# Optimization experiments

Hardware: AMD Instinct MI355X
Metric: run time of the kernel (lower is better)

The kernel has to match this reference:

```python
import jax, jax.numpy as jnp
import numpy as np

NUM_GRAPHS = 16


def gat_layer(x, src, dst, n, W, a_s, a_d, b):
    # PyG GATConv, concat=False (mean over heads), negative_slope=0.2
    H, C = a_s.shape
    h = (x @ W).reshape(x.shape[0], H, C)            # [N,H,C]
    es = jnp.einsum('nhc,hc->nh', h, a_s)            # alpha_src per node
    ed = jnp.einsum('nhc,hc->nh', h, a_d)            # alpha_dst per node
    e = jax.nn.leaky_relu(es[src] + ed[dst], 0.2)    # [E,H]
    m = jax.ops.segment_max(e, dst, num_segments=n)
    m = jnp.where(jnp.isfinite(m), m, 0.0)
    p = jnp.exp(e - m[dst])
    denom = jax.ops.segment_sum(p, dst, num_segments=n)
    alpha = p / (denom[dst] + 1e-16)                 # segment softmax over in-edges
    out = jax.ops.segment_sum(h[src] * alpha[..., None], dst, num_segments=n)  # [N,H,C]
    return out.mean(axis=1) + b


def _forward(x, edge_index, batch,
             W_e0, a_s_e0, a_d_e0, b_e0, W_e1, a_s_e1, a_d_e1, b_e1,
             W_d0, a_s_d0, a_d_d0, b_d0, W_d1, a_s_d1, a_d_d1, b_d1,
             g_w1, g_b1, g_w2, g_b2):
    n = x.shape[0]
    loop = jnp.arange(n, dtype=edge_index.dtype)     # PyG add_self_loops=True
    src = jnp.concatenate([edge_index[0], loop])
    dst = jnp.concatenate([edge_index[1], loop])
    # encoder (dropout inert in eval)
    h = jax.nn.relu(gat_layer(x, src, dst, n, W_e0, a_s_e0, a_d_e0, b_e0))
    h = gat_layer(h, src, dst, n, W_e1, a_s_e1, a_d_e1, b_e1)
    # GlobalAttention pooling: gate MLP -> segment softmax over graphs -> scatter sum
    gate = (jax.nn.relu(h @ g_w1 + g_b1) @ g_w2 + g_b2)[:, 0]   # [N]
    gm = jax.ops.segment_max(gate, batch, num_segments=NUM_GRAPHS)
    gm = jnp.where(jnp.isfinite(gm), gm, 0.0)
    p = jnp.exp(gate - gm[batch])
    att = p / (jax.ops.segment_sum(p, batch, num_segments=NUM_GRAPHS)[batch] + 1e-16)
    pooled = jax.ops.segment_sum(att[:, None] * h, batch, num_segments=NUM_GRAPHS)
    h = pooled[batch]                                # broadcast pooled back to nodes
    # decoder (heads=1)
    h = jax.nn.relu(gat_layer(h, src, dst, n, W_d0, a_s_d0, a_d_d0, b_d0))
    return gat_layer(h, src, dst, n, W_d1, a_s_d1, a_d_d1, b_d1)


def setup_inputs() -> dict:
    key = jax.random.key(0)
    ks = jax.random.split(key, 24)
    N, E, Din, H, C = 50000, 250000, 128, 8, 64
    def w(k, shape, fan_in):
        return (jax.random.normal(k, shape, jnp.float32) / np.sqrt(fan_in)).astype(jnp.float32)
    return {
        'x': jax.random.normal(ks[0], (N, Din), jnp.float32),
        'edge_index': jax.random.randint(ks[1], (2, E), 0, N, dtype=jnp.int32),
        'batch': jnp.sort(jax.random.randint(ks[2], (N,), 0, NUM_GRAPHS, dtype=jnp.int32)),
        'W_e0': w(ks[3], (Din, H * C), Din), 'a_s_e0': w(ks[4], (H, C), C), 'a_d_e0': w(ks[5], (H, C), C), 'b_e0': w(ks[6], (C,), C),
        'W_e1': w(ks[7], (C, H * C), C), 'a_s_e1': w(ks[8], (H, C), C), 'a_d_e1': w(ks[9], (H, C), C), 'b_e1': w(ks[10], (C,), C),
        'W_d0': w(ks[11], (C, C), C), 'a_s_d0': w(ks[12], (1, C), C), 'a_d_d0': w(ks[13], (1, C), C), 'b_d0': w(ks[14], (C,), C),
        'W_d1': w(ks[15], (C, Din), C), 'a_s_d1': w(ks[16], (1, Din), Din), 'a_d_d1': w(ks[17], (1, Din), Din), 'b_d1': w(ks[18], (Din,), Din),
        'g_w1': w(ks[19], (C, C), C), 'g_b1': w(ks[20], (C,), C), 'g_w2': w(ks[21], (C, 1), C), 'g_b2': w(ks[22], (1,), C),
    }


def reference(x, edge_index, batch,
              W_e0, a_s_e0, a_d_e0, b_e0, W_e1, a_s_e1, a_d_e1, b_e1,
              W_d0, a_s_d0, a_d_d0, b_d0, W_d1, a_s_d1, a_d_d1, b_d1,
              g_w1, g_b1, g_w2, g_b2):
    return _forward(x, edge_index, batch,
                    W_e0, a_s_e0, a_d_e0, b_e0, W_e1, a_s_e1, a_d_e1, b_e1,
                    W_d0, a_s_d0, a_d_d0, b_d0, W_d1, a_s_d1, a_d_d1, b_d1,
                    g_w1, g_b1, g_w2, g_b2)
```

## Files before the change

### kernel.cpp

```cpp
#include <hip/hip_runtime.h>
#include <hip/hip_fp16.h>
#include <math.h>

#define TB 256

typedef _Float16 half8v __attribute__((ext_vector_type(8)));
typedef float float4v __attribute__((ext_vector_type(4)));

static __device__ __forceinline__ int edge_src(const int* ei, int E, int e) {
    return (e < E) ? ei[e] : (e - E);
}
static __device__ __forceinline__ int edge_dst(const int* ei, int E, int e) {
    return (e < E) ? ei[E + e] : (e - E);
}

__global__ void csr_count(const int* __restrict__ ei, int E, int Etot, int* __restrict__ cnt) {
    int e = blockIdx.x * blockDim.x + threadIdx.x;
    if (e >= Etot) return;
    atomicAdd(&cnt[edge_dst(ei, E, e)], 1);
}

__global__ __launch_bounds__(256) void scan_phase1(const int* __restrict__ cnt,
                                                   int* __restrict__ incl,
                                                   int* __restrict__ bsum, int n) {
// ... 20 lines not shown
        __syncthreads();
    }
    if (t < nb) bsum[t] = v;
}

__global__ __launch_bounds__(256) void scan_phase3(const int* __restrict__ incl,
                                                   const int* __restrict__ bsum,
                                                   int* __restrict__ off, int n) {
    int i = blockIdx.x * 256 + threadIdx.x;
    if (i < n) off[i + 1] = incl[i] + (blockIdx.x ? bsum[blockIdx.x - 1] : 0);
    if (i == 0) off[0] = 0;
}

__global__ void csr_fill(const int* __restrict__ ei, int E, int Etot,
                         const int* __restrict__ off, int* __restrict__ cur,
                         int* __restrict__ esrc) {
    int e = blockIdx.x * blockDim.x + threadIdx.x;
    if (e >= Etot) return;
    int d = edge_dst(ei, E, e);
    int pos = atomicAdd(&cur[d], 1);
    esrc[off[d] + pos] = edge_src(ei, E, e);
}

__global__ void prep_weights(const float* __restrict__ W_e0, const float* __restrict__ g_w1,
                             const float* __restrict__ W_e1, const float* __restrict__ W_d1,
                             __half* __restrict__ wt_e0, __half* __restrict__ wt_g1,
                             __half* __restrict__ wst_e1, __half* __restrict__ wst_d1) {
    int i = blockIdx.x * blockDim.x + threadIdx.x;
    if (i < 65536) {
        int nn = i / 128, kk = i % 128;
        wt_e0[i] = __float2half(W_e0[kk * 512 + nn]);
    } else if (i < 69632) {
        int j = i - 65536;
        int nn = j / 64, kk = j % 64;
        wt_g1[j] = __float2half(g_w1[kk * 64 + nn]);
    } else if (i < 102400) {
        int j = i - 69632;
        int c = j / 512, rem = j % 512;
        int h = rem / 64, k = rem % 64;
        wst_e1[j] = __float2half(W_e1[(size_t)k * 512 + h * 64 + c]);
    } else if (i < 110592) {
        int j = i - 102400;
        int c = j / 64, k = j % 64;
        wst_d1[j] = __float2half(W_d1[(size_t)k * 128 + c]);
    }
}

__global__ void prep_ws(const float* __restrict__ W_e0, const float* __restrict__ a_s_e0,
                        const float* __restrict__ a_d_e0,
                        const float* __restrict__ W_e1, const float* __restrict__ a_s_e1,
                        const float* __restrict__ a_d_e1,
                        const float* __restrict__ W_d1, const float* __restrict__ a_s_d1,
                        const float* __restrict__ a_d_d1,
                        float* __restrict__ ws_e0, float* __restrict__ wd_e0,
                        float* __restrict__ ws_e1, float* __restrict__ wd_e1,
                        float* __restrict__ ws_d1, float* __restrict__ wd_d1) {
    int i = blockIdx.x * blockDim.x + threadIdx.x;
    const float* W; const float* as_; const float* ad_;
    float* ws; float* wd;
    int K, H, C, j;
    if (i < 1024) { j = i; K = 128; H = 8; C = 64; W = W_e0; as_ = a_s_e0; ad_ = a_d_e0; ws = ws_e0; wd = wd_e0; }
    else if (i < 1536) { j = i - 1024; K = 64; H = 8; C = 64; W = W_e1; as_ = a_s_e1; ad_ = a_d_e1; ws = ws_e1; wd = wd_e1; }
    else if (i < 1600) { j = i - 1536; K = 64; H = 1; C = 128; W = W_d1; as_ = a_s_d1; ad_ = a_d_d1; ws = ws_d1; wd = wd_d1; }
    else return;
    int h = j / K, k = j % K;
    const float* wrow = W + (size_t)k * H * C + h * C;
    float s = 0.f, d = 0.f;
    for (int c = 0; c < C; ++c) {
        s += wrow[c] * as_[h * C + c];
        d += wrow[c] * ad_[h * C + c];
    }
    ws[j] = s;
    wd[j] = d;
}

__global__ __launch_bounds__(256) void gemm_mfma_wide(const __half* __restrict__ A,
                                                      const __half* __restrict__ BT,
                                                      __half* __restrict__ C,
                                                      int M, int N) {
    constexpr int K = 128, KP = 136;
    __shared__ __align__(16) __half As[64 * KP];
    __shared__ __align__(16) __half Bs[128 * KP];
    int tid = threadIdx.x;
    int bm = blockIdx.y * 64, bn = blockIdx.x * 128;
    for (int idx = tid; idx < 64 * 16; idx += 256) {
        int row = idx >> 4, ko = (idx & 15) * 8;
        uint4 v = make_uint4(0u, 0u, 0u, 0u);
        int gr = bm + row;
        if (gr < M) v = *(const uint4*)(A + (size_t)gr * K + ko);
        *(uint4*)(&As[row * KP + ko]) = v;
    }
    for (int idx = tid; idx < 128 * 16; idx += 256) {
        int row = idx >> 4, ko = (idx & 15) * 8;
        *(uint4*)(&Bs[row * KP + ko]) = *(const uint4*)(BT + (size_t)(bn + row) * K + ko);
    }
    __syncthreads();
    int wv_ = tid >> 6, l = tid & 63;
    int lr = l & 15, g = l >> 4;
    float4v acc[8] = {{0,0,0,0},{0,0,0,0},{0,0,0,0},{0,0,0,0},
                      {0,0,0,0},{0,0,0,0},{0,0,0,0},{0,0,0,0}};
    const __half* ap = &As[(16 * wv_ + lr) * KP + 8 * g];
    const __half* bp = &Bs[lr * KP + 8 * g];
#pragma unroll
    for (int k0 = 0; k0 < K; k0 += 32) {
        half8v af = *reinterpret_cast<const half8v*>(ap + k0);
#pragma unroll
        for (int nt = 0; nt < 8; ++nt) {
            half8v bf = *reinterpret_cast<const half8v*>(bp + nt * 16 * KP + k0);
            acc[nt] = __builtin_amdgcn_mfma_f32_16x16x32_f16(af, bf, acc[nt], 0, 0, 0);
        }
    }
#pragma unroll
    for (int nt = 0; nt < 8; ++nt) {
#pragma unroll
        for (int r = 0; r < 4; ++r) {
            int grow = bm + 16 * wv_ + 4 * g + r;
            if (grow < M)
                C[(size_t)grow * N + bn + nt * 16 + lr] = __float2half(acc[nt][r]);
        }
    }
}

template <int K, int H>
__global__ __launch_bounds__(256) void scores_cast_nt(const float* __restrict__ X,
                                                      __half* __restrict__ X16,
                                                      const float* __restrict__ ws,
                                                      const float* __restrict__ wd,
                                                      float* __restrict__ es,
                                                      float* __restrict__ ed, int N) {
    int n = blockIdx.x * blockDim.x + threadIdx.x;
    if (n >= N) return;
    const float* row = X + (size_t)n * K;
    __half* row16 = X16 + (size_t)n * K;
    float s[H] = {}, d[H] = {};
#pragma unroll
    for (int k0 = 0; k0 < K; k0 += 8) {
        float4 a0 = *(const float4*)(row + k0);
        float4 a1 = *(const float4*)(row + k0 + 4);
        float a[8] = {a0.x, a0.y, a0.z, a0.w, a1.x, a1.y, a1.z, a1.w};
        __half2 h0 = __floats2half2_rn(a[0], a[1]);
        __half2 h1 = __floats2half2_rn(a[2], a[3]);
        __half2 h2 = __floats2half2_rn(a[4], a[5]);
        __half2 h3 = __floats2half2_rn(a[6], a[7]);
        uint4 pk;
        pk.x = *(unsigned*)&h0; pk.y = *(unsigned*)&h1;
        pk.z = *(unsigned*)&h2; pk.w = *(unsigned*)&h3;
        *(uint4*)(row16 + k0) = pk;
#pragma unroll
        for (int h = 0; h < H; ++h)
#pragma unroll
            for (int q = 0; q < 8; ++q) {
                s[h] += a[q] * ws[h * K + k0 + q];
                d[h] += a[q] * wd[h * K + k0 + q];
            }
    }
#pragma unroll
    for (int h = 0; h < H; ++h) {
        es[(size_t)n * H + h] = s[h];
        ed[(size_t)n * H + h] = d[h];
    }
}

template <int K, int H>
__global__ __launch_bounds__(256) void scores_nt(const __half* __restrict__ A,
                                                 const float* __restrict__ ws,
                                                 const float* __restrict__ wd,
                                                 float* __restrict__ es,
                                                 float* __restrict__ ed, int N) {
    int n = blockIdx.x * blockDim.x + threadIdx.x;
    if (n >= N) return;
// ... 10 lines not shown
        for (int h = 0; h < H; ++h)
#pragma unroll
            for (int q = 0; q < 8; ++q) {
                s[h] += a[q] * ws[h * K + k0 + q];
                d[h] += a[q] * wd[h * K + k0 + q];
            }
    }
#pragma unroll
    for (int h = 0; h < H; ++h) {
        es[(size_t)n * H + h] = s[h];
        ed[(size_t)n * H + h] = d[h];
    }
}

template <bool RELU>
__global__ __launch_bounds__(256) void gat_gather_h8(const __half* __restrict__ hsrc,
                                                     const float* __restrict__ es,
                                                     const float* __restrict__ ed,
                                                     const int* __restrict__ off,
                                                     const int* __restrict__ esrc,
                                                     const float* __restrict__ bias,
                                                     __half* __restrict__ out, int N) {
    constexpr int HC = 512;
    int n = (blockIdx.x * blockDim.x + threadIdx.x) >> 6;
    int lane = threadIdx.x & 63;
    if (n >= N) return;
    int hd = lane >> 3;
    int k8 = lane >> 3, h8 = lane & 7;
    int j0 = off[n], j1 = off[n + 1];

    float edl = ed[(size_t)n * 8 + h8];

    float acc[8] = {};
    float denacc = 0.f;
    for (int j = j0; j < j1; j += 8) {
        int jj = j + k8;
        int jc = (jj < j1) ? jj : (j1 - 1);
        int sidx = esrc[jc];
        float v = es[(size_t)sidx * 8 + h8] + edl;
        v = (v > 0.f) ? v : 0.2f * v;
        float pm = (jj < j1) ? expf(v) : 0.f;
        denacc += pm;
        uint4 rw[8];
#pragma unroll
        for (int k = 0; k < 8; ++k) {
            int sb = __shfl(sidx, k * 8);
            rw[k] = *(const uint4*)(hsrc + (size_t)sb * HC + 8 * lane);
        }
#pragma unroll
        for (int k = 0; k < 8; ++k) {
            float a = __shfl(pm, k * 8 + hd);
            const __half* hv = (const __half*)&rw[k];
#pragma unroll
            for (int q = 0; q < 8; ++q) acc[q] += a * __half2float(hv[q]);
        }
    }

    float den = denacc;
#pragma unroll
    for (int o = 8; o < 64; o <<= 1) den += __shfl_xor(den, o);
    float dv = __shfl(den, hd) + 1e-16f;

#pragma unroll
    for (int q = 0; q < 8; ++q) acc[q] /= dv;
#pragma unroll
    for (int o = 8; o < 64; o <<= 1)
#pragma unroll
        for (int q = 0; q < 8; ++q) acc[q] += __shfl_xor(acc[q], o);

    if (lane < 8) {
        int cbase = 8 * lane;
        float r[8];
#pragma unroll
        for (int q = 0; q < 8; ++q) {
            float o2 = acc[q] * 0.125f + bias[cbase + q];
            if (RELU) o2 = fmaxf(o2, 0.f);
            r[q] = o2;
        }
        __half2 p0 = __floats2half2_rn(r[0], r[1]);
        __half2 p1 = __floats2half2_rn(r[2], r[3]);
        __half2 p2 = __floats2half2_rn(r[4], r[5]);
        __half2 p3 = __floats2half2_rn(r[6], r[7]);
        uint4 pk;
        pk.x = *(unsigned*)&p0; pk.y = *(unsigned*)&p1;
        pk.z = *(unsigned*)&p2; pk.w = *(unsigned*)&p3;
        *(uint4*)(out + (size_t)n * 64 + cbase) = pk;
    }
}

__global__ __launch_bounds__(256) void gat_gather_zh8(const __half* __restrict__ A,
                                                      const float* __restrict__ es,
                                                      const float* __restrict__ ed,
                                                      const int* __restrict__ off,
                                                      const int* __restrict__ esrc,
                                                      __half* __restrict__ z, int N) {
    int n = (blockIdx.x * blockDim.x + threadIdx.x) >> 6;
    int lane = threadIdx.x & 63;
    if (n >= N) return;
    int h = lane >> 3, q = lane & 7;
    int j0 = off[n], j1 = off[n + 1];
    float edv = ed[(size_t)n * 8 + h];

    float acc[8] = {};
    float den = 0.f;
    int j = j0;
    for (; j + 1 < j1; j += 2) {
        int s0 = esrc[j], s1 = esrc[j + 1];
        float v0 = es[(size_t)s0 * 8 + h] + edv;
        float v1 = es[(size_t)s1 * 8 + h] + edv;
        v0 = (v0 > 0.f) ? v0 : 0.2f * v0;
        v1 = (v1 > 0.f) ? v1 : 0.2f * v1;
        float p0 = expf(v0), p1 = expf(v1);
        den += p0 + p1;
        uint4 r0 = *(const uint4*)(A + (size_t)s0 * 64 + 8 * q);
        uint4 r1 = *(const uint4*)(A + (size_t)s1 * 64 + 8 * q);
        const __half* h0 = (const __half*)&r0;
        const __half* h1 = (const __half*)&r1;
#pragma unroll
        for (int k = 0; k < 8; ++k)
            acc[k] += p0 * __half2float(h0[k]) + p1 * __half2float(h1[k]);
    }
    if (j < j1) {
        int s0 = esrc[j];
        float v0 = es[(size_t)s0 * 8 + h] + edv;
        v0 = (v0 > 0.f) ? v0 : 0.2f * v0;
        float p0 = expf(v0);
        den += p0;
        uint4 r0 = *(const uint4*)(A + (size_t)s0 * 64 + 8 * q);
        const __half* h0 = (const __half*)&r0;
#pragma unroll
        for (int k = 0; k < 8; ++k) acc[k] += p0 * __half2float(h0[k]);
    }

    float inv = 1.f / ((den + 1e-16f) * 8.f);
    float r[8];
#pragma unroll
    for (int k = 0; k < 8; ++k) r[k] = acc[k] * inv;
    __half2 p0 = __floats2half2_rn(r[0], r[1]);
    __half2 p1 = __floats2half2_rn(r[2], r[3]);
    __half2 p2 = __floats2half2_rn(r[4], r[5]);
    __half2 p3 = __floats2half2_rn(r[6], r[7]);
    uint4 pk;
    pk.x = *(unsigned*)&p0; pk.y = *(unsigned*)&p1;
    pk.z = *(unsigned*)&p2; pk.w = *(unsigned*)&p3;
    *(uint4*)(z + (size_t)n * 512 + h * 64 + 8 * q) = pk;
}

__global__ __launch_bounds__(256) void gat_gather_z8(const __half* __restrict__ A,
                                                     const float* __restrict__ es,
                                                     const float* __restrict__ ed,
                                                     const int* __restrict__ off,
                                                     const int* __restrict__ esrc,
                                                     __half* __restrict__ z, int N) {
    int n = (blockIdx.x * blockDim.x + threadIdx.x) >> 6;
    int lane = threadIdx.x & 63;
    if (n >= N) return;
    int k8 = lane >> 3, q8 = lane & 7;
    int j0 = off[n], j1 = off[n + 1];
    float edv = ed[n];

    float acc[8] = {};
    float denacc = 0.f;
    for (int j = j0; j < j1; j += 8) {
        int jj = j + k8;
        int jc = (jj < j1) ? jj : (j1 - 1);
        int sidx = esrc[jc];
        float v = es[sidx] + edv;
        v = (v > 0.f) ? v : 0.2f * v;
        float pm = (jj < j1) ? expf(v) : 0.f;
        denacc += pm;
        uint4 rw = *(const uint4*)(A + (size_t)sidx * 64 + 8 * q8);
        const __half* hv = (const __half*)&rw;
#pragma unroll
        for (int q = 0; q < 8; ++q) acc[q] += pm * __half2float(hv[q]);
    }

    float den = denacc;
#pragma unroll
    for (int o = 8; o < 64; o <<= 1) {
        den += __shfl_xor(den, o);
#pragma unroll
        for (int q = 0; q < 8; ++q) acc[q] += __shfl_xor(acc[q], o);
    }
    float inv = 1.f / (den + 1e-16f);
    if (lane < 8) {
        float r[8];
#pragma unroll
        for (int q = 0; q < 8; ++q) r[q] = acc[q] * inv;
        __half2 p0 = __floats2half2_rn(r[0], r[1]);
        __half2 p1 = __floats2half2_rn(r[2], r[3]);
        __half2 p2 = __floats2half2_rn(r[4], r[5]);
        __half2 p3 = __floats2half2_rn(r[6], r[7]);
        uint4 pk;
        pk.x = *(unsigned*)&p0; pk.y = *(unsigned*)&p1;
        pk.z = *(unsigned*)&p2; pk.w = *(unsigned*)&p3;
        *(uint4*)(z + (size_t)n * 64 + 8 * lane) = pk;
    }
}

template <int KK, typename OUTT, bool RELU>
__global__ __launch_bounds__(256) void gemm_kt(const __half* __restrict__ A,
                                               const __half* __restrict__ BT,
                                               const float* __restrict__ bias,
                                               OUTT* __restrict__ C,
                                               int M, int Nout) {
    __shared__ __align__(16) __half As[64 * 72];
    __shared__ __align__(16) __half Bs[64 * 72];
    int tid = threadIdx.x;
    int bm = blockIdx.y * 64, bn = blockIdx.x * 64;
    int wv = tid >> 6, l = tid & 63, lr = l & 15, g = l >> 4;
    float4v acc[4] = {{0.f, 0.f, 0.f, 0.f}, {0.f, 0.f, 0.f, 0.f},
                      {0.f, 0.f, 0.f, 0.f}, {0.f, 0.f, 0.f, 0.f}};
    for (int kc = 0; kc < KK; kc += 64) {
        __syncthreads();
        for (int idx = tid; idx < 512; idx += 256) {
            int row = idx >> 3, ko = (idx & 7) * 8;
            uint4 v = make_uint4(0u, 0u, 0u, 0u);
            int gr = bm + row;
            if (gr < M) v = *(const uint4*)(A + (size_t)gr * KK + kc + ko);
// ... 22 lines not shown
                float c = acc[nt][r] + b;
                if (RELU) c = fmaxf(c, 0.f);
                if constexpr (sizeof(OUTT) == 2)
                    C[(size_t)grow * Nout + bn + nt * 16 + lr] = __float2half(c);
                else
                    C[(size_t)grow * Nout + bn + nt * 16 + lr] = c;
            }
        }
    }
}

__global__ __launch_bounds__(256) void gat_gather_d08s(const float* __restrict__ hsrc,
                                                       const float* __restrict__ es16,
                                                       const float* __restrict__ ed16,
                                                       const int* __restrict__ off,
                                                       const int* __restrict__ esrc,
                                                       const int* __restrict__ batch,
                                                       const float* __restrict__ bias,
                                                       const float* __restrict__ ws2,
                                                       const float* __restrict__ wd2,
                                                       __half* __restrict__ out,
                                                       float* __restrict__ es2,
                                                       float* __restrict__ ed2, int N) {
    int n = (blockIdx.x * blockDim.x + threadIdx.x) >> 6;
    int lane = threadIdx.x & 63;
    if (n >= N) return;
    int k8 = lane >> 3, q8 = lane & 7;
    int j0 = off[n], j1 = off[n + 1];
    float edv = ed16[batch[n]];

    float acc[8] = {};
    float denacc = 0.f;
    for (int j = j0; j < j1; j += 8) {
        int jj = j + k8;
        int jc = (jj < j1) ? jj : (j1 - 1);
        int g = batch[esrc[jc]];
        float v = es16[g] + edv;
        v = (v > 0.f) ? v : 0.2f * v;
        float pm = (jj < j1) ? expf(v) : 0.f;
        denacc += pm;
        const float* row = hsrc + (size_t)g * 64 + 8 * q8;
        float4 r0 = *(const float4*)row;
        float4 r1 = *(const float4*)(row + 4);
        acc[0] += pm * r0.x; acc[1] += pm * r0.y;
        acc[2] += pm * r0.z; acc[3] += pm * r0.w;
        acc[4] += pm * r1.x; acc[5] += pm * r1.y;
        acc[6] += pm * r1.z; acc[7] += pm * r1.w;
    }

    float den = denacc;
#pragma unroll
    for (int o = 8; o < 64; o <<= 1) {
        den += __shfl_xor(den, o);
#pragma unroll
        for (int q = 0; q < 8; ++q) acc[q] += __shfl_xor(acc[q], o);
    }
    float inv = 1.f / (den + 1e-16f);
    if (lane < 8) {
        int cbase = 8 * lane;
        float r[8];
#pragma unroll
        for (int q = 0; q < 8; ++q) r[q] = fmaxf(acc[q] * inv + bias[cbase + q], 0.f);
        __half2 p0 = __floats2half2_rn(r[0], r[1]);
        __half2 p1 = __floats2half2_rn(r[2], r[3]);
        __half2 p2 = __floats2half2_rn(r[4], r[5]);
        __half2 p3 = __floats2half2_rn(r[6], r[7]);
        uint4 pk;
        pk.x = *(unsigned*)&p0; pk.y = *(unsigned*)&p1;
        pk.z = *(unsigned*)&p2; pk.w = *(unsigned*)&p3;
        *(uint4*)(out + (size_t)n * 64 + cbase) = pk;
        float ps = 0.f, pd = 0.f;
#pragma unroll
        for (int q = 0; q < 8; ++q) {
            ps += r[q] * ws2[cbase + q];
            pd += r[q] * wd2[cbase + q];
        }
#pragma unroll
        for (int o = 1; o < 8; o <<= 1) {
            ps += __shfl_xor(ps, o);
            pd += __shfl_xor(pd, o);
        }
        if (lane == 0) {
            es2[n] = ps;
            ed2[n] = pd;
        }
    }
}

__global__ __launch_bounds__(256) void gate_pool_mfma(const __half* __restrict__ A,
                                                      const __half* __restrict__ BT,
                                                      const float* __restrict__ b1,
                                                      const float* __restrict__ w2,
                                                      const float* __restrict__ b2,
                                                      const int* __restrict__ batch,
                                                      float* __restrict__ pg,
                                                      float* __restrict__ gden,
                                                      float* __restrict__ pooled, int M) {
    constexpr int KP = 72;
    __shared__ __align__(16) __half As[64 * KP];
    __shared__ __align__(16) __half Bs[64 * KP];
    __shared__ float part[16];
    __shared__ float sp[64];
    __shared__ int sb[64];
    int tid = threadIdx.x;
    if (tid < 16) part[tid] = 0.f;
    int bm = blockIdx.x * 64;
    for (int idx = tid; idx < 512; idx += 256) {
// ... 76 lines not shown
__global__ void dec_prep(const float* __restrict__ pooled, const float* __restrict__ gden,
                         const float* __restrict__ Wd0, const float* __restrict__ asd,
                         const float* __restrict__ add, float* __restrict__ hd016,
                         float* __restrict__ es16, float* __restrict__ ed16) {
    int g = blockIdx.x;
    int lane = threadIdx.x;
    float pn = pooled[g * 64 + lane] / (gden[g] + 1e-16f);
    float o = 0.f;
    for (int c = 0; c < 64; ++c) o += __shfl(pn, c) * Wd0[c * 64 + lane];
    hd016[g * 64 + lane] = o;
    float s = o * asd[lane], d = o * add[lane];
#pragma unroll
    for (int off = 32; off; off >>= 1) {
        s += __shfl_xor(s, off);
        d += __shfl_xor(d, off);
    }
    if (lane == 0) {
        es16[g] = s;
        ed16[g] = d;
    }
}

static inline int cdiv(int a, int b) { return (a + b - 1) / b; }

extern "C" void kernel_launch(void* const* d_in, const int* in_sizes, int n_in,
                              void* d_out, int out_size, void* d_ws, size_t ws_size,
                              hipStream_t stream) {
    const float* x      = (const float*)d_in[0];
    const int*   ei     = (const int*)  d_in[1];
    const int*   batch  = (const int*)  d_in[2];
    const float* W_e0   = (const float*)d_in[3];
    const float* a_s_e0 = (const float*)d_in[4];
    const float* a_d_e0 = (const float*)d_in[5];
    const float* b_e0   = (const float*)d_in[6];
    const float* W_e1   = (const float*)d_in[7];
    const float* a_s_e1 = (const float*)d_in[8];
    const float* a_d_e1 = (const float*)d_in[9];
    const float* b_e1   = (const float*)d_in[10];
    const float* W_d0   = (const float*)d_in[11];
    const float* a_s_d0 = (const float*)d_in[12];
    const float* a_d_d0 = (const float*)d_in[13];
    const float* b_d0   = (const float*)d_in[14];
    const float* W_d1   = (const float*)d_in[15];
    const float* a_s_d1 = (const float*)d_in[16];
    const float* a_d_d1 = (const float*)d_in[17];
    const float* b_d1   = (const float*)d_in[18];
    const float* g_w1   = (const float*)d_in[19];
    const float* g_b1   = (const float*)d_in[20];
    const float* g_w2   = (const float*)d_in[21];
    const float* g_b2   = (const float*)d_in[22];

    const int N    = in_sizes[2];
    const int E    = in_sizes[1] / 2;
    const int Etot = E + N;
    const int Din  = in_sizes[0] / N;

    char* w = (char*)d_ws;
    size_t o = 0;
    auto alloc = [&](size_t bytes) -> void* {
        void* p = w + o;
        o = (o + bytes + 255) & ~(size_t)255;
        return p;
    };
    __half*   h16    = (__half*)  alloc((size_t)N * 512 * 2);
    __half*   x16    = (__half*)  alloc((size_t)N * Din * 2);
    __half*   bufA   = (__half*)  alloc((size_t)N * 64 * 2);
    __half*   bufB   = (__half*)  alloc((size_t)N * 64 * 2);
    __half*   wt_e0  = (__half*)  alloc((size_t)512 * 128 * 2);
    __half*   wst_e1 = (__half*)  alloc((size_t)64 * 512 * 2);
    __half*   wst_d1 = (__half*)  alloc((size_t)128 * 64 * 2);
    __half*   wt_g1  = (__half*)  alloc((size_t)64 * 64 * 2);
    float*    ws_e0  = (float*)   alloc(8 * 128 * 4);
    float*    wd_e0  = (float*)   alloc(8 * 128 * 4);
    float*    ws_e1  = (float*)   alloc(8 * 64 * 4);
    float*    wd_e1  = (float*)   alloc(8 * 64 * 4);
    float*    ws_d1  = (float*)   alloc(64 * 4);
    float*    wd_d1  = (float*)   alloc(64 * 4);
    float*    es     = (float*)   alloc((size_t)N * 8 * 4);
    float*    ed     = (float*)   alloc((size_t)N * 8 * 4);
    float*    pg     = (float*)   alloc((size_t)N * 4);
    int*      off    = (int*)     alloc((size_t)(N + 1) * 4);
    int*      cnt    = (int*)     alloc((size_t)N * 4);
    int*      esrc   = (int*)     alloc((size_t)Etot * 4);
    int*      bsum   = (int*)     alloc(256 * 4);
    float*    gden   = (float*)   alloc(16 * 4);
    float*    pooled = (float*)   alloc(16 * 64 * 4);
    float*    hd016  = (float*)   alloc(16 * 64 * 4);
    float*    es16   = (float*)   alloc(16 * 4);
    float*    ed16   = (float*)   alloc(16 * 4);
    (void)ws_size; (void)n_in; (void)out_size;

    const int nodeWaveGrid = cdiv(N, 4);
    const int nodeThreadGrid = cdiv(N, TB);
    const int edgeGrid     = cdiv(Etot, TB);
    const int scanBlocks   = cdiv(N, 256);

    hipMemsetAsync(cnt, 0, (size_t)N * 4, stream);
    csr_count<<<edgeGrid, TB, 0, stream>>>(ei, E, Etot, cnt);
    scan_phase1<<<scanBlocks, 256, 0, stream>>>(cnt, esrc , bsum, N);
    scan_phase2<<<1, 256, 0, stream>>>(bsum, scanBlocks);
    scan_phase3<<<scanBlocks, 256, 0, stream>>>(esrc, bsum, off, N);
    hipMemsetAsync(cnt, 0, (size_t)N * 4, stream);
    csr_fill<<<edgeGrid, TB, 0, stream>>>(ei, E, Etot, off, cnt, esrc);

    prep_weights<<<cdiv(110592, TB), TB, 0, stream>>>(W_e0, g_w1, W_e1, W_d1,
                                                      wt_e0, wt_g1, wst_e1, wst_d1);
    prep_ws<<<cdiv(1600, TB), TB, 0, stream>>>(W_e0, a_s_e0, a_d_e0,
                                               W_e1, a_s_e1, a_d_e1,
                                               W_d1, a_s_d1, a_d_d1,
                                               ws_e0, wd_e0, ws_e1, wd_e1, ws_d1, wd_d1);

    scores_cast_nt<128, 8><<<nodeThreadGrid, TB, 0, stream>>>(x, x16, ws_e0, wd_e0, es, ed, N);
    {
        dim3 grid(512 / 128, cdiv(N, 64));
        gemm_mfma_wide<<<grid, TB, 0, stream>>>(x16, wt_e0, h16, N, 512);
    }
    gat_gather_h8<true><<<nodeWaveGrid, TB, 0, stream>>>(
        h16, es, ed, off, esrc, b_e0, bufA, N);

    scores_nt<64, 8><<<nodeThreadGrid, TB, 0, stream>>>(bufA, ws_e1, wd_e1, es, ed, N);
    gat_gather_zh8<<<nodeWaveGrid, TB, 0, stream>>>(bufA, es, ed, off, esrc, h16 , N);
    {
        dim3 grid(1, cdiv(N, 64));
        gemm_kt<512, __half, false><<<grid, TB, 0, stream>>>(h16 , wst_e1, b_e1, bufB, N, 64);
    }

    hipMemsetAsync(gden, 0, 256 + 16 * 64 * 4, stream);
    gate_pool_mfma<<<cdiv(N, 64), TB, 0, stream>>>(bufB, wt_g1, g_b1, g_w2, g_b2,
                                                   batch, pg, gden, pooled, N);
    dec_prep<<<16, 64, 0, stream>>>(pooled, gden, W_d0, a_s_d0, a_d_d0, hd016, es16, ed16);

    gat_gather_d08s<<<nodeWaveGrid, TB, 0, stream>>>(
        hd016, es16, ed16, off, esrc, batch, b_d0, ws_d1, wd_d1, bufA, es, ed, N);

    gat_gather_z8<<<nodeWaveGrid, TB, 0, stream>>>(bufA, es, ed, off, esrc, h16 , N);
    {
        dim3 grid(2, cdiv(N, 64));
        gemm_kt<64, float, false><<<grid, TB, 0, stream>>>(h16 , wst_d1, b_d1, (float*)d_out, N, 128);
    }
}
```

Baseline: 327.5 us.

## Fuse weight prep, fold x cast into GEMM, persistent gather kernels

Merges prep_weights and prep_ws into a single prep_all launch. Drops the separate fp16 copy of x by converting fp32 to fp16 inside the first GEMM's shared-memory load, and scores now read only fp32. Converts the four gather kernels to persistent grid-stride loops over nodes with a fixed grid of 2048 blocks, and combines the two counter memsets into one by adding a separate cur buffer. This removes launches, a full N×128 fp16 write/read and a memset, at the cost of more global bytes read per GEMM tile and possible load imbalance in the persistent gathers.

```diff
diff --git a/kernel.cpp b/kernel.cpp
--- a/kernel.cpp
+++ b/kernel.cpp
@@ -66,10 +66,16 @@
     esrc[off[d] + pos] = edge_src(ei, E, e);
 }
 
-__global__ void prep_weights(const float* __restrict__ W_e0, const float* __restrict__ g_w1,
-                             const float* __restrict__ W_e1, const float* __restrict__ W_d1,
-                             __half* __restrict__ wt_e0, __half* __restrict__ wt_g1,
-                             __half* __restrict__ wst_e1, __half* __restrict__ wst_d1) {
+__global__ void prep_all(const float* __restrict__ W_e0, const float* __restrict__ g_w1,
+                         const float* __restrict__ W_e1, const float* __restrict__ W_d1,
+                         const float* __restrict__ a_s_e0, const float* __restrict__ a_d_e0,
+                         const float* __restrict__ a_s_e1, const float* __restrict__ a_d_e1,
+                         const float* __restrict__ a_s_d1, const float* __restrict__ a_d_d1,
+                         __half* __restrict__ wt_e0, __half* __restrict__ wt_g1,
+                         __half* __restrict__ wst_e1, __half* __restrict__ wst_d1,
+                         float* __restrict__ ws_e0, float* __restrict__ wd_e0,
+                         float* __restrict__ ws_e1, float* __restrict__ wd_e1,
+                         float* __restrict__ ws_d1, float* __restrict__ wd_d1) {
     int i = blockIdx.x * blockDim.x + threadIdx.x;
     if (i < 65536) {
         int nn = i / 128, kk = i % 128;
@@ -87,41 +93,30 @@
         int j = i - 102400;
         int c = j / 64, k = j % 64;
         wst_d1[j] = __float2half(W_d1[(size_t)k * 128 + c]);
-    }
-}
-
-__global__ void prep_ws(const float* __restrict__ W_e0, const float* __restrict__ a_s_e0,
-                        const float* __restrict__ a_d_e0,
-                        const float* __restrict__ W_e1, const float* __restrict__ a_s_e1,
-                        const float* __restrict__ a_d_e1,
-                        const float* __restrict__ W_d1, const float* __restrict__ a_s_d1,
-                        const float* __restrict__ a_d_d1,
-                        float* __restrict__ ws_e0, float* __restrict__ wd_e0,
-                        float* __restrict__ ws_e1, float* __restrict__ wd_e1,
-                        float* __restrict__ ws_d1, float* __restrict__ wd_d1) {
-    int i = blockIdx.x * blockDim.x + threadIdx.x;
-    const float* W; const float* as_; const float* ad_;
-    float* ws; float* wd;
-    int K, H, C, j;
-    if (i < 1024) { j = i; K = 128; H = 8; C = 64; W = W_e0; as_ = a_s_e0; ad_ = a_d_e0; ws = ws_e0; wd = wd_e0; }
-    else if (i < 1536) { j = i - 1024; K = 64; H = 8; C = 64; W = W_e1; as_ = a_s_e1; ad_ = a_d_e1; ws = ws_e1; wd = wd_e1; }
-    else if (i < 1600) { j = i - 1536; K = 64; H = 1; C = 128; W = W_d1; as_ = a_s_d1; ad_ = a_d_d1; ws = ws_d1; wd = wd_d1; }
-    else return;
-    int h = j / K, k = j % K;
-    const float* wrow = W + (size_t)k * H * C + h * C;
-    float s = 0.f, d = 0.f;
-    for (int c = 0; c < C; ++c) {
-        s += wrow[c] * as_[h * C + c];
-        d += wrow[c] * ad_[h * C + c];
-    }
-    ws[j] = s;
-    wd[j] = d;
-}
-
-__global__ __launch_bounds__(256) void gemm_mfma_wide(const __half* __restrict__ A,
-                                                      const __half* __restrict__ BT,
-                                                      __half* __restrict__ C,
-                                                      int M, int N) {
+    } else if (i < 112192) {
+        int jj = i - 110592;
+        const float* W; const float* as_; const float* ad_;
+        float* ws; float* wd;
+        int K, H, C, j;
+        if (jj < 1024) { j = jj; K = 128; H = 8; C = 64; W = W_e0; as_ = a_s_e0; ad_ = a_d_e0; ws = ws_e0; wd = wd_e0; }
+        else if (jj < 1536) { j = jj - 1024; K = 64; H = 8; C = 64; W = W_e1; as_ = a_s_e1; ad_ = a_d_e1; ws = ws_e1; wd = wd_e1; }
+        else { j = jj - 1536; K = 64; H = 1; C = 128; W = W_d1; as_ = a_s_d1; ad_ = a_d_d1; ws = ws_d1; wd = wd_d1; }
+        int h = j / K, k = j % K;
+        const float* wrow = W + (size_t)k * H * C + h * C;
+        float s = 0.f, d = 0.f;
+        for (int c = 0; c < C; ++c) {
+            s += wrow[c] * as_[h * C + c];
+            d += wrow[c] * ad_[h * C + c];
+        }
+        ws[j] = s;
+        wd[j] = d;
+    }
+}
+
+__global__ __launch_bounds__(256) void gemm_mfma_wide_f32(const float* __restrict__ A,
+                                                          const __half* __restrict__ BT,
+                                                          __half* __restrict__ C,
+                                                          int M, int N) {
     constexpr int K = 128, KP = 136;
     __shared__ __align__(16) __half As[64 * KP];
     __shared__ __align__(16) __half Bs[128 * KP];
@@ -129,10 +124,19 @@
     int bm = blockIdx.y * 64, bn = blockIdx.x * 128;
     for (int idx = tid; idx < 64 * 16; idx += 256) {
         int row = idx >> 4, ko = (idx & 15) * 8;
-        uint4 v = make_uint4(0u, 0u, 0u, 0u);
         int gr = bm + row;
-        if (gr < M) v = *(const uint4*)(A + (size_t)gr * K + ko);
-        *(uint4*)(&As[row * KP + ko]) = v;
+        uint4 pk = make_uint4(0u, 0u, 0u, 0u);
+        if (gr < M) {
+            float4 a0 = *(const float4*)(A + (size_t)gr * K + ko);
+            float4 a1 = *(const float4*)(A + (size_t)gr * K + ko + 4);
+            __half2 h0 = __floats2half2_rn(a0.x, a0.y);
+            __half2 h1 = __floats2half2_rn(a0.z, a0.w);
+            __half2 h2 = __floats2half2_rn(a1.x, a1.y);
+            __half2 h3 = __floats2half2_rn(a1.z, a1.w);
+            pk.x = *(unsigned*)&h0; pk.y = *(unsigned*)&h1;
+            pk.z = *(unsigned*)&h2; pk.w = *(unsigned*)&h3;
+        }
+        *(uint4*)(&As[row * KP + ko]) = pk;
     }
     for (int idx = tid; idx < 128 * 16; idx += 256) {
         int row = idx >> 4, ko = (idx & 15) * 8;
@@ -166,30 +170,20 @@
 }
 
 template <int K, int H>
-__global__ __launch_bounds__(256) void scores_cast_nt(const float* __restrict__ X,
-                                                      __half* __restrict__ X16,
-                                                      const float* __restrict__ ws,
-                                                      const float* __restrict__ wd,
-                                                      float* __restrict__ es,
-                                                      float* __restrict__ ed, int N) {
+__global__ __launch_bounds__(256) void scores_f32(const float* __restrict__ X,
+                                                  const float* __restrict__ ws,
+                                                  const float* __restrict__ wd,
+                                                  float* __restrict__ es,
+                                                  float* __restrict__ ed, int N) {
     int n = blockIdx.x * blockDim.x + threadIdx.x;
     if (n >= N) return;
     const float* row = X + (size_t)n * K;
-    __half* row16 = X16 + (size_t)n * K;
     float s[H] = {}, d[H] = {};
 #pragma unroll
     for (int k0 = 0; k0 < K; k0 += 8) {
         float4 a0 = *(const float4*)(row + k0);
         float4 a1 = *(const float4*)(row + k0 + 4);
         float a[8] = {a0.x, a0.y, a0.z, a0.w, a1.x, a1.y, a1.z, a1.w};
-        __half2 h0 = __floats2half2_rn(a[0], a[1]);
-        __half2 h1 = __floats2half2_rn(a[2], a[3]);
-        __half2 h2 = __floats2half2_rn(a[4], a[5]);
-        __half2 h3 = __floats2half2_rn(a[6], a[7]);
-        uint4 pk;
-        pk.x = *(unsigned*)&h0; pk.y = *(unsigned*)&h1;
-        pk.z = *(unsigned*)&h2; pk.w = *(unsigned*)&h3;
-        *(uint4*)(row16 + k0) = pk;
 #pragma unroll
         for (int h = 0; h < H; ++h)
 #pragma unroll
@@ -246,61 +240,122 @@
                                                      const float* __restrict__ bias,
                                                      __half* __restrict__ out, int N) {
     constexpr int HC = 512;
-    int n = (blockIdx.x * blockDim.x + threadIdx.x) >> 6;
+    int wid = (blockIdx.x * blockDim.x + threadIdx.x) >> 6;
+    int nw = (gridDim.x * blockDim.x) >> 6;
     int lane = threadIdx.x & 63;
-    if (n >= N) return;
     int hd = lane >> 3;
     int k8 = lane >> 3, h8 = lane & 7;
-    int j0 = off[n], j1 = off[n + 1];
-
-    float edl = ed[(size_t)n * 8 + h8];
-
-    float acc[8] = {};
-    float denacc = 0.f;
-    for (int j = j0; j < j1; j += 8) {
-        int jj = j + k8;
-        int jc = (jj < j1) ? jj : (j1 - 1);
-        int sidx = esrc[jc];
-        float v = es[(size_t)sidx * 8 + h8] + edl;
-        v = (v > 0.f) ? v : 0.2f * v;
-        float pm = (jj < j1) ? expf(v) : 0.f;
-        denacc += pm;
-        uint4 rw[8];
-#pragma unroll
-        for (int k = 0; k < 8; ++k) {
-            int sb = __shfl(sidx, k * 8);
-            rw[k] = *(const uint4*)(hsrc + (size_t)sb * HC + 8 * lane);
-        }
-#pragma unroll
-        for (int k = 0; k < 8; ++k) {
-            float a = __shfl(pm, k * 8 + hd);
-            const __half* hv = (const __half*)&rw[k];
-#pragma unroll
-            for (int q = 0; q < 8; ++q) acc[q] += a * __half2float(hv[q]);
-        }
-    }
-
-    float den = denacc;
-#pragma unroll
-    for (int o = 8; o < 64; o <<= 1) den += __shfl_xor(den, o);
-    float dv = __shfl(den, hd) + 1e-16f;
-
-#pragma unroll
-    for (int q = 0; q < 8; ++q) acc[q] /= dv;
-#pragma unroll
-    for (int o = 8; o < 64; o <<= 1)
-#pragma unroll
-        for (int q = 0; q < 8; ++q) acc[q] += __shfl_xor(acc[q], o);
-
-    if (lane < 8) {
-        int cbase = 8 * lane;
+
+    for (int n = wid; n < N; n += nw) {
+        int j0 = off[n], j1 = off[n + 1];
+        float edl = ed[(size_t)n * 8 + h8];
+        float acc[8] = {};
+        float denacc = 0.f;
+        for (int j = j0; j < j1; j += 8) {
+            int jj = j + k8;
+            int jc = (jj < j1) ? jj : (j1 - 1);
+            int sidx = esrc[jc];
+            float v = es[(size_t)sidx * 8 + h8] + edl;
+            v = (v > 0.f) ? v : 0.2f * v;
+            float pm = (jj < j1) ? expf(v) : 0.f;
+            denacc += pm;
+            uint4 rw[8];
+#pragma unroll
+            for (int k = 0; k < 8; ++k) {
+                int sb = __shfl(sidx, k * 8);
+                rw[k] = *(const uint4*)(hsrc + (size_t)sb * HC + 8 * lane);
+            }
+#pragma unroll
+            for (int k = 0; k < 8; ++k) {
+                float a = __shfl(pm, k * 8 + hd);
+                const __half* hv = (const __half*)&rw[k];
+#pragma unroll
+                for (int q = 0; q < 8; ++q) acc[q] += a * __half2float(hv[q]);
+            }
+        }
+
+        float den = denacc;
+#pragma unroll
+        for (int o = 8; o < 64; o <<= 1) den += __shfl_xor(den, o);
+        float dv = __shfl(den, hd) + 1e-16f;
+
+#pragma unroll
+        for (int q = 0; q < 8; ++q) acc[q] /= dv;
+#pragma unroll
+        for (int o = 8; o < 64; o <<= 1)
+#pragma unroll
+            for (int q = 0; q < 8; ++q) acc[q] += __shfl_xor(acc[q], o);
+
+        if (lane < 8) {
+            int cbase = 8 * lane;
+            float r[8];
+#pragma unroll
+            for (int q = 0; q < 8; ++q) {
+                float o2 = acc[q] * 0.125f + bias[cbase + q];
+                if (RELU) o2 = fmaxf(o2, 0.f);
+                r[q] = o2;
+            }
+            __half2 p0 = __floats2half2_rn(r[0], r[1]);
+            __half2 p1 = __floats2half2_rn(r[2], r[3]);
+            __half2 p2 = __floats2half2_rn(r[4], r[5]);
+            __half2 p3 = __floats2half2_rn(r[6], r[7]);
+            uint4 pk;
+            pk.x = *(unsigned*)&p0; pk.y = *(unsigned*)&p1;
+            pk.z = *(unsigned*)&p2; pk.w = *(unsigned*)&p3;
+            *(uint4*)(out + (size_t)n * 64 + cbase) = pk;
+        }
+    }
+}
+
+__global__ __launch_bounds__(256) void gat_gather_zh8(const __half* __restrict__ A,
+                                                      const float* __restrict__ es,
+                                                      const float* __restrict__ ed,
+                                                      const int* __restrict__ off,
+                                                      const int* __restrict__ esrc,
+                                                      __half* __restrict__ z, int N) {
+    int wid = (blockIdx.x * blockDim.x + threadIdx.x) >> 6;
+    int nw = (gridDim.x * blockDim.x) >> 6;
+    int lane = threadIdx.x & 63;
+    int h = lane >> 3, q = lane & 7;
+
+    for (int n = wid; n < N; n += nw) {
+        int j0 = off[n], j1 = off[n + 1];
+        float edv = ed[(size_t)n * 8 + h];
+        float acc[8] = {};
+        float den = 0.f;
+        int j = j0;
+        for (; j + 1 < j1; j += 2) {
+            int s0 = esrc[j], s1 = esrc[j + 1];
+            float v0 = es[(size_t)s0 * 8 + h] + edv;
+            float v1 = es[(size_t)s1 * 8 + h] + edv;
+            v0 = (v0 > 0.f) ? v0 : 0.2f * v0;
+            v1 = (v1 > 0.f) ? v1 : 0.2f * v1;
+            float p0 = expf(v0), p1 = expf(v1);
+            den += p0 + p1;
+            uint4 r0 = *(const uint4*)(A + (size_t)s0 * 64 + 8 * q);
+            uint4 r1 = *(const uint4*)(A + (size_t)s1 * 64 + 8 * q);
+            const __half* h0 = (const __half*)&r0;
+            const __half* h1 = (const __half*)&r1;
+#pragma unroll
+            for (int k = 0; k < 8; ++k)
+                acc[k] += p0 * __half2float(h0[k]) + p1 * __half2float(h1[k]);
+        }
+        if (j < j1) {
+            int s0 = esrc[j];
+            float v0 = es[(size_t)s0 * 8 + h] + edv;
+            v0 = (v0 > 0.f) ? v0 : 0.2f * v0;
+            float p0 = expf(v0);
+            den += p0;
+            uint4 r0 = *(const uint4*)(A + (size_t)s0 * 64 + 8 * q);
+            const __half* h0 = (const __half*)&r0;
+#pragma unroll
+            for (int k = 0; k < 8; ++k) acc[k] += p0 * __half2float(h0[k]);
+        }
+
+        float inv = 1.f / ((den + 1e-16f) * 8.f);
         float r[8];
 #pragma unroll
-        for (int q = 0; q < 8; ++q) {
-            float o2 = acc[q] * 0.125f + bias[cbase + q];
-            if (RELU) o2 = fmaxf(o2, 0.f);
-            r[q] = o2;
-        }
+        for (int k = 0; k < 8; ++k) r[k] = acc[k] * inv;
         __half2 p0 = __floats2half2_rn(r[0], r[1]);
         __half2 p1 = __floats2half2_rn(r[2], r[3]);
         __half2 p2 = __floats2half2_rn(r[4], r[5]);
@@ -308,66 +363,8 @@
         uint4 pk;
         pk.x = *(unsigned*)&p0; pk.y = *(unsigned*)&p1;
         pk.z = *(unsigned*)&p2; pk.w = *(unsigned*)&p3;
-        *(uint4*)(out + (size_t)n * 64 + cbase) = pk;
-    }
-}
-
-__global__ __launch_bounds__(256) void gat_gather_zh8(const __half* __restrict__ A,
-                                                      const float* __restrict__ es,
-                                                      const float* __restrict__ ed,
-                                                      const int* __restrict__ off,
-                                                      const int* __restrict__ esrc,
-                                                      __half* __restrict__ z, int N) {
-    int n = (blockIdx.x * blockDim.x + threadIdx.x) >> 6;
-    int lane = threadIdx.x & 63;
-    if (n >= N) return;
-    int h = lane >> 3, q = lane & 7;
-    int j0 = off[n], j1 = off[n + 1];
-    float edv = ed[(size_t)n * 8 + h];
-
-    float acc[8] = {};
-    float den = 0.f;
-    int j = j0;
-    for (; j + 1 < j1; j += 2) {
-        int s0 = esrc[j], s1 = esrc[j + 1];
-        float v0 = es[(size_t)s0 * 8 + h] + edv;
-        float v1 = es[(size_t)s1 * 8 + h] + edv;
-        v0 = (v0 > 0.f) ? v0 : 0.2f * v0;
-        v1 = (v1 > 0.f) ? v1 : 0.2f * v1;
-        float p0 = expf(v0), p1 = expf(v1);
-        den += p0 + p1;
-        uint4 r0 = *(const uint4*)(A + (size_t)s0 * 64 + 8 * q);
-        uint4 r1 = *(const uint4*)(A + (size_t)s1 * 64 + 8 * q);
-        const __half* h0 = (const __half*)&r0;
-        const __half* h1 = (const __half*)&r1;
-#pragma unroll
-        for (int k = 0; k < 8; ++k)
-            acc[k] += p0 * __half2float(h0[k]) + p1 * __half2float(h1[k]);
-    }
-    if (j < j1) {
-        int s0 = esrc[j];
-        float v0 = es[(size_t)s0 * 8 + h] + edv;
-        v0 = (v0 > 0.f) ? v0 : 0.2f * v0;
-        float p0 = expf(v0);
-        den += p0;
-        uint4 r0 = *(const uint4*)(A + (size_t)s0 * 64 + 8 * q);
-        const __half* h0 = (const __half*)&r0;
-#pragma unroll
-        for (int k = 0; k < 8; ++k) acc[k] += p0 * __half2float(h0[k]);
-    }
-
-    float inv = 1.f / ((den + 1e-16f) * 8.f);
-    float r[8];
-#pragma unroll
-    for (int k = 0; k < 8; ++k) r[k] = acc[k] * inv;
-    __half2 p0 = __floats2half2_rn(r[0], r[1]);
-    __half2 p1 = __floats2half2_rn(r[2], r[3]);
-    __half2 p2 = __floats2half2_rn(r[4], r[5]);
-    __half2 p3 = __floats2half2_rn(r[6], r[7]);
-    uint4 pk;
-    pk.x = *(unsigned*)&p0; pk.y = *(unsigned*)&p1;
-    pk.z = *(unsigned*)&p2; pk.w = *(unsigned*)&p3;
-    *(uint4*)(z + (size_t)n * 512 + h * 64 + 8 * q) = pk;
+        *(uint4*)(z + (size_t)n * 512 + h * 64 + 8 * q) = pk;
+    }
 }
 
 __global__ __launch_bounds__(256) void gat_gather_z8(const __half* __restrict__ A,
@@ -376,49 +373,51 @@
                                                      const int* __restrict__ off,
                                                      const int* __restrict__ esrc,
                                                      __half* __restrict__ z, int N) {
-    int n = (blockIdx.x * blockDim.x + threadIdx.x) >> 6;
+    int wid = (blockIdx.x * blockDim.x + threadIdx.x) >> 6;
+    int nw = (gridDim.x * blockDim.x) >> 6;
     int lane = threadIdx.x & 63;
-    if (n >= N) return;
     int k8 = lane >> 3, q8 = lane & 7;
-    int j0 = off[n], j1 = off[n + 1];
-    float edv = ed[n];
-
-    float acc[8] = {};
-    float denacc = 0.f;
-    for (int j = j0; j < j1; j += 8) {
-        int jj = j + k8;
-        int jc = (jj < j1) ? jj : (j1 - 1);
-        int sidx = esrc[jc];
-        float v = es[sidx] + edv;
-        v = (v > 0.f) ? v : 0.2f * v;
-        float pm = (jj < j1) ? expf(v) : 0.f;
-        denacc += pm;
-        uint4 rw = *(const uint4*)(A + (size_t)sidx * 64 + 8 * q8);
-        const __half* hv = (const __half*)&rw;
-#pragma unroll
-        for (int q = 0; q < 8; ++q) acc[q] += pm * __half2float(hv[q]);
-    }
-
-    float den = denacc;
-#pragma unroll
-    for (int o = 8; o < 64; o <<= 1) {
-        den += __shfl_xor(den, o);
-#pragma unroll
-        for (int q = 0; q < 8; ++q) acc[q] += __shfl_xor(acc[q], o);
-    }
-    float inv = 1.f / (den + 1e-16f);
-    if (lane < 8) {
-        float r[8];
-#pragma unroll
-        for (int q = 0; q < 8; ++q) r[q] = acc[q] * inv;
-        __half2 p0 = __floats2half2_rn(r[0], r[1]);
-        __half2 p1 = __floats2half2_rn(r[2], r[3]);
-        __half2 p2 = __floats2half2_rn(r[4], r[5]);
-        __half2 p3 = __floats2half2_rn(r[6], r[7]);
-        uint4 pk;
-        pk.x = *(unsigned*)&p0; pk.y = *(unsigned*)&p1;
-        pk.z = *(unsigned*)&p2; pk.w = *(unsigned*)&p3;
-        *(uint4*)(z + (size_t)n * 64 + 8 * lane) = pk;
+
+    for (int n = wid; n < N; n += nw) {
+        int j0 = off[n], j1 = off[n + 1];
+        float edv = ed[n];
+        float acc[8] = {};
+        float denacc = 0.f;
+        for (int j = j0; j < j1; j += 8) {
+            int jj = j + k8;
+            int jc = (jj < j1) ? jj : (j1 - 1);
+            int sidx = esrc[jc];
+            float v = es[sidx] + edv;
+            v = (v > 0.f) ? v : 0.2f * v;
+            float pm = (jj < j1) ? expf(v) : 0.f;
+            denacc += pm;
+            uint4 rw = *(const uint4*)(A + (size_t)sidx * 64 + 8 * q8);
+            const __half* hv = (const __half*)&rw;
+#pragma unroll
+            for (int q = 0; q < 8; ++q) acc[q] += pm * __half2float(hv[q]);
+        }
+
+        float den = denacc;
+#pragma unroll
+        for (int o = 8; o < 64; o <<= 1) {
+            den += __shfl_xor(den, o);
+#pragma unroll
+            for (int q = 0; q < 8; ++q) acc[q] += __shfl_xor(acc[q], o);
+        }
+        float inv = 1.f / (den + 1e-16f);
+        if (lane < 8) {
+            float r[8];
+#pragma unroll
+            for (int q = 0; q < 8; ++q) r[q] = acc[q] * inv;
+            __half2 p0 = __floats2half2_rn(r[0], r[1]);
+            __half2 p1 = __floats2half2_rn(r[2], r[3]);
+            __half2 p2 = __floats2half2_rn(r[4], r[5]);
+            __half2 p3 = __floats2half2_rn(r[6], r[7]);
+            uint4 pk;
+            pk.x = *(unsigned*)&p0; pk.y = *(unsigned*)&p1;
+            pk.z = *(unsigned*)&p2; pk.w = *(unsigned*)&p3;
+            *(uint4*)(z + (size_t)n * 64 + 8 * lane) = pk;
+        }
     }
 }
 
@@ -487,67 +486,69 @@
                                                        __half* __restrict__ out,
                                                        float* __restrict__ es2,
                                                        float* __restrict__ ed2, int N) {
-    int n = (blockIdx.x * blockDim.x + threadIdx.x) >> 6;
+    int wid = (blockIdx.x * blockDim.x + threadIdx.x) >> 6;
+    int nw = (gridDim.x * blockDim.x) >> 6;
     int lane = threadIdx.x & 63;
-    if (n >= N) return;
     int k8 = lane >> 3, q8 = lane & 7;
-    int j0 = off[n], j1 = off[n + 1];
-    float edv = ed16[batch[n]];
-
-    float acc[8] = {};
-    float denacc = 0.f;
-    for (int j = j0; j < j1; j += 8) {
-        int jj = j + k8;
-        int jc = (jj < j1) ? jj : (j1 - 1);
-        int g = batch[esrc[jc]];
-        float v = es16[g] + edv;
-        v = (v > 0.f) ? v : 0.2f * v;
-        float pm = (jj < j1) ? expf(v) : 0.f;
-        denacc += pm;
-        const float* row = hsrc + (size_t)g * 64 + 8 * q8;
-        float4 r0 = *(const float4*)row;
-        float4 r1 = *(const float4*)(row + 4);
-        acc[0] += pm * r0.x; acc[1] += pm * r0.y;
-        acc[2] += pm * r0.z; acc[3] += pm * r0.w;
-        acc[4] += pm * r1.x; acc[5] += pm * r1.y;
-        acc[6] += pm * r1.z; acc[7] += pm * r1.w;
-    }
-
-    float den = denacc;
-#pragma unroll
-    for (int o = 8; o < 64; o <<= 1) {
-        den += __shfl_xor(den, o);
-#pragma unroll
-        for (int q = 0; q < 8; ++q) acc[q] += __shfl_xor(acc[q], o);
-    }
-    float inv = 1.f / (den + 1e-16f);
-    if (lane < 8) {
-        int cbase = 8 * lane;
-        float r[8];
-#pragma unroll
-        for (int q = 0; q < 8; ++q) r[q] = fmaxf(acc[q] * inv + bias[cbase + q], 0.f);
-        __half2 p0 = __floats2half2_rn(r[0], r[1]);
-        __half2 p1 = __floats2half2_rn(r[2], r[3]);
-        __half2 p2 = __floats2half2_rn(r[4], r[5]);
-        __half2 p3 = __floats2half2_rn(r[6], r[7]);
-        uint4 pk;
-        pk.x = *(unsigned*)&p0; pk.y = *(unsigned*)&p1;
-        pk.z = *(unsigned*)&p2; pk.w = *(unsigned*)&p3;
-        *(uint4*)(out + (size_t)n * 64 + cbase) = pk;
-        float ps = 0.f, pd = 0.f;
-#pragma unroll
-        for (int q = 0; q < 8; ++q) {
-            ps += r[q] * ws2[cbase + q];
-            pd += r[q] * wd2[cbase + q];
-        }
-#pragma unroll
-        for (int o = 1; o < 8; o <<= 1) {
-            ps += __shfl_xor(ps, o);
-            pd += __shfl_xor(pd, o);
-        }
-        if (lane == 0) {
-            es2[n] = ps;
-            ed2[n] = pd;
+
+    for (int n = wid; n < N; n += nw) {
+        int j0 = off[n], j1 = off[n + 1];
+        float edv = ed16[batch[n]];
+        float acc[8] = {};
+        float denacc = 0.f;
+        for (int j = j0; j < j1; j += 8) {
+            int jj = j + k8;
+            int jc = (jj < j1) ? jj : (j1 - 1);
+            int g = batch[esrc[jc]];
+            float v = es16[g] + edv;
+            v = (v > 0.f) ? v : 0.2f * v;
+            float pm = (jj < j1) ? expf(v) : 0.f;
+            denacc += pm;
+            const float* row = hsrc + (size_t)g * 64 + 8 * q8;
+            float4 r0 = *(const float4*)row;
+            float4 r1 = *(const float4*)(row + 4);
+            acc[0] += pm * r0.x; acc[1] += pm * r0.y;
+            acc[2] += pm * r0.z; acc[3] += pm * r0.w;
+            acc[4] += pm * r1.x; acc[5] += pm * r1.y;
+            acc[6] += pm * r1.z; acc[7] += pm * r1.w;
+        }
+
+        float den = denacc;
+#pragma unroll
+        for (int o = 8; o < 64; o <<= 1) {
+            den += __shfl_xor(den, o);
+#pragma unroll
+            for (int q = 0; q < 8; ++q) acc[q] += __shfl_xor(acc[q], o);
+        }
+        float inv = 1.f / (den + 1e-16f);
+        if (lane < 8) {
+            int cbase = 8 * lane;
+            float r[8];
+#pragma unroll
+            for (int q = 0; q < 8; ++q) r[q] = fmaxf(acc[q] * inv + bias[cbase + q], 0.f);
+            __half2 p0 = __floats2half2_rn(r[0], r[1]);
+            __half2 p1 = __floats2half2_rn(r[2], r[3]);
+            __half2 p2 = __floats2half2_rn(r[4], r[5]);
+            __half2 p3 = __floats2half2_rn(r[6], r[7]);
+            uint4 pk;
+            pk.x = *(unsigned*)&p0; pk.y = *(unsigned*)&p1;
+            pk.z = *(unsigned*)&p2; pk.w = *(unsigned*)&p3;
+            *(uint4*)(out + (size_t)n * 64 + cbase) = pk;
+            float ps = 0.f, pd = 0.f;
+#pragma unroll
+            for (int q = 0; q < 8; ++q) {
+                ps += r[q] * ws2[cbase + q];
+                pd += r[q] * wd2[cbase + q];
+            }
+#pragma unroll
+            for (int o = 1; o < 8; o <<= 1) {
+                ps += __shfl_xor(ps, o);
+                pd += __shfl_xor(pd, o);
+            }
+            if (lane == 0) {
+                es2[n] = ps;
+                ed2[n] = pd;
+            }
         }
     }
 }
@@ -670,6 +671,7 @@
 }
 
 static inline int cdiv(int a, int b) { return (a + b - 1) / b; }
+static inline size_t al256(size_t b) { return (b + 255) & ~(size_t)255; }
 
 extern "C" void kernel_launch(void* const* d_in, const int* in_sizes, int n_in,
                               void* d_out, int out_size, void* d_ws, size_t ws_size,
@@ -707,11 +709,10 @@
     size_t o = 0;
     auto alloc = [&](size_t bytes) -> void* {
         void* p = w + o;
-        o = (o + bytes + 255) & ~(size_t)255;
+        o = al256(o + bytes);
         return p;
     };
     __half*   h16    = (__half*)  alloc((size_t)N * 512 * 2);
-    __half*   x16    = (__half*)  alloc((size_t)N * Din * 2);
     __half*   bufA   = (__half*)  alloc((size_t)N * 64 * 2);
     __half*   bufB   = (__half*)  alloc((size_t)N * 64 * 2);
     __half*   wt_e0  = (__half*)  alloc((size_t)512 * 128 * 2);
@@ -729,6 +730,7 @@
     float*    pg     = (float*)   alloc((size_t)N * 4);
     int*      off    = (int*)     alloc((size_t)(N + 1) * 4);
     int*      cnt    = (int*)     alloc((size_t)N * 4);
+    int*      cur    = (int*)     alloc((size_t)N * 4);
     int*      esrc   = (int*)     alloc((size_t)Etot * 4);
     int*      bsum   = (int*)     alloc(256 * 4);
     float*    gden   = (float*)   alloc(16 * 4);
@@ -738,50 +740,48 @@
     float*    ed16   = (float*)   alloc(16 * 4);
     (void)ws_size; (void)n_in; (void)out_size;
 
-    const int nodeWaveGrid = cdiv(N, 4);
+    const int persistGrid = 2048;
     const int nodeThreadGrid = cdiv(N, TB);
     const int edgeGrid     = cdiv(Etot, TB);
     const int scanBlocks   = cdiv(N, 256);
 
-    hipMemsetAsync(cnt, 0, (size_t)N * 4, stream);
+    hipMemsetAsync(cnt, 0, al256((size_t)N * 4) + (size_t)N * 4, stream);
     csr_count<<<edgeGrid, TB, 0, stream>>>(ei, E, Etot, cnt);
     scan_phase1<<<scanBlocks, 256, 0, stream>>>(cnt, esrc , bsum, N);
     scan_phase2<<<1, 256, 0, stream>>>(bsum, scanBlocks);
     scan_phase3<<<scanBlocks, 256, 0, stream>>>(esrc, bsum, off, N);
-    hipMemsetAsync(cnt, 0, (size_t)N * 4, stream);
-    csr_fill<<<edgeGrid, TB, 0, stream>>>(ei, E, Etot, off, cnt, esrc);
-
-    prep_weights<<<cdiv(110592, TB), TB, 0, stream>>>(W_e0, g_w1, W_e1, W_d1,
-                                                      wt_e0, wt_g1, wst_e1, wst_d1);
-    prep_ws<<<cdiv(1600, TB), TB, 0, stream>>>(W_e0, a_s_e0, a_d_e0,
-                                               W_e1, a_s_e1, a_d_e1,
-                                               W_d1, a_s_d1, a_d_d1,
-                                               ws_e0, wd_e0, ws_e1, wd_e1, ws_d1, wd_d1);
-
-    scores_cast_nt<128, 8><<<nodeThreadGrid, TB, 0, stream>>>(x, x16, ws_e0, wd_e0, es, ed, N);
+    csr_fill<<<edgeGrid, TB, 0, stream>>>(ei, E, Etot, off, cur, esrc);
+
+    prep_all<<<cdiv(112192, TB), TB, 0, stream>>>(W_e0, g_w1, W_e1, W_d1,
+                                                  a_s_e0, a_d_e0, a_s_e1, a_d_e1,
+                                                  a_s_d1, a_d_d1,
+                                                  wt_e0, wt_g1, wst_e1, wst_d1,
+                                                  ws_e0, wd_e0, ws_e1, wd_e1, ws_d1, wd_d1);
+
+    scores_f32<128, 8><<<nodeThreadGrid, TB, 0, stream>>>(x, ws_e0, wd_e0, es, ed, N);
     {
         dim3 grid(512 / 128, cdiv(N, 64));
-        gemm_mfma_wide<<<grid, TB, 0, stream>>>(x16, wt_e0, h16, N, 512);
-    }
-    gat_gather_h8<true><<<nodeWaveGrid, TB, 0, stream>>>(
+        gemm_mfma_wide_f32<<<grid, TB, 0, stream>>>(x, wt_e0, h16, N, 512);
+    }
+    gat_gather_h8<true><<<persistGrid, TB, 0, stream>>>(
         h16, es, ed, off, esrc, b_e0, bufA, N);
 
     scores_nt<64, 8><<<nodeThreadGrid, TB, 0, stream>>>(bufA, ws_e1, wd_e1, es, ed, N);
-    gat_gather_zh8<<<nodeWaveGrid, TB, 0, stream>>>(bufA, es, ed, off, esrc, h16 , N);
+    gat_gather_zh8<<<persistGrid, TB, 0, stream>>>(bufA, es, ed, off, esrc, h16 , N);
     {
         dim3 grid(1, cdiv(N, 64));
         gemm_kt<512, __half, false><<<grid, TB, 0, stream>>>(h16 , wst_e1, b_e1, bufB, N, 64);
     }
 
-    hipMemsetAsync(gden, 0, 256 + 16 * 64 * 4, stream);
+    hipMemsetAsync(gden, 0, al256(16 * 4) + 16 * 64 * 4, stream);
     gate_pool_mfma<<<cdiv(N, 64), TB, 0, stream>>>(bufB, wt_g1, g_b1, g_w2, g_b2,
                                                    batch, pg, gden, pooled, N);
     dec_prep<<<16, 64, 0, stream>>>(pooled, gden, W_d0, a_s_d0, a_d_d0, hd016, es16, ed16);
 
-    gat_gather_d08s<<<nodeWaveGrid, TB, 0, stream>>>(
+    gat_gather_d08s<<<persistGrid, TB, 0, stream>>>(
         hd016, es16, ed16, off, esrc, batch, b_d0, ws_d1, wd_d1, bufA, es, ed, N);
 
-    gat_gather_z8<<<nodeWaveGrid, TB, 0, stream>>>(bufA, es, ed, off, esrc, h16 , N);
+    gat_gather_z8<<<persistGrid, TB, 0, stream>>>(bufA, es, ed, off, esrc, h16 , N);
     {
         dim3 grid(2, cdiv(N, 64));
         gemm_kt<64, float, false><<<grid, TB, 0, stream>>>(h16 , wst_d1, b_d1, (float*)d_out, N, 128);
```

After: 322.7 us. No clear change (-1.4%).
